# Kernel tuning notes

Hardware: AMD Instinct MI355X
Metric: run time of the kernel (lower is better)

The kernel has to match this reference:

```python
import jax, jax.numpy as jnp
import numpy as np
from jax import lax

SHIFT = 32  # shift_range from init
EPS_NORM = 1e-12
EPS_MASK = 1e-6


def _l2_normalize_flat(x):
    # F.normalize(x.reshape(B,-1)): per-sample L2 normalize with eps 1e-12
    B = x.shape[0]
    flat = x.reshape(B, -1)
    n = jnp.linalg.norm(flat, axis=1, keepdims=True)
    return (flat / jnp.maximum(n, EPS_NORM)).reshape(x.shape)


def setup_inputs() -> dict:
    key = jax.random.key(0)
    k1, k2 = jax.random.split(key)
    grd_feature = jax.random.normal(k1, (8, 32, 32, 32), dtype=jnp.float32)
    sat_feature = jax.random.normal(k2, (8, 32, 128, 128), dtype=jnp.float32)
    return {"grd_feature": grd_feature, "sat_feature": sat_feature, "test_method": 1}


def reference(grd_feature, sat_feature, test_method):
    # test_method == 1 path (default); test_method in {0,1} only differ in divisor
    M, C, H_s, W_s = sat_feature.shape
    N, _, H, W = grd_feature.shape
    kH = min(H, H_s - 2 * SHIFT)
    kW = min(W, W_s - 2 * SHIFT)

    # center-crop ground template to (kH, kW) and L2-normalize per sample
    gh0, gw0 = H // 2 - kH // 2, W // 2 - kW // 2
    grd = grd_feature[:, :, gh0:gh0 + 2 * (kH // 2), gw0:gw0 + 2 * (kW // 2)]
    N_, _, H_k, W_k = grd.shape
    grd = _l2_normalize_flat(grd)

    # center-crop satellite to search region and L2-normalize per sample
    sh0 = H_s // 2 - SHIFT - kH // 2
    sw0 = W_s // 2 - SHIFT - kW // 2
    sat = sat_feature[:, :, sh0:sh0 + 2 * (SHIFT + kH // 2), sw0:sw0 + 2 * (SHIFT + kW // 2)]
    _, _, H_i, W_i = sat.shape
    sat = _l2_normalize_flat(sat)

    # all-pairs cross-correlation: corr[m, n, y, x] (torch grouped-conv on repeated sat
    # is equivalent to a plain VALID conv of sat with all N ground filters)
    corr = lax.conv_general_dilated(
        sat, grd, window_strides=(1, 1), padding='VALID',
        dimension_numbers=('NCHW', 'OIHW', 'NCHW'))  # [M, N, Ho, Wo]
    Ho, Wo = corr.shape[2], corr.shape[3]

    # sliding-window sum of |sat|^2 (avg_pool with divisor_override=1, summed over C)
    s2 = jnp.sum(sat * sat, axis=1)  # [M, H_i, W_i]
    partical = lax.reduce_window(s2, jnp.float32(0), lax.add,
                                 (1, H_k, W_k), (1, 1, 1), 'VALID')  # [M, Ho, Wo]
    if test_method == 0:
        denom = jnp.sqrt(partical)
    else:
        denom = partical
    corr = corr / jnp.maximum(denom[:, None], EPS_NORM)

    similarity_matrix = jnp.max(corr, axis=(2, 3))  # [M, N]

    # diagonal pairs (m == n): peak localization
    diag = jnp.diagonal(corr, axis1=0, axis2=1)        # [Ho, Wo, M]
    diag = jnp.transpose(diag, (2, 0, 1)).reshape(M, -1)
    max_index = jnp.argmax(diag, axis=-1)
    pos_h = max_index // Wo
    pos_w = max_index % Wo

    grd_mask = (jnp.abs(jnp.sum(grd, axis=1)) > EPS_MASK).astype(jnp.float32)  # [N, H_k, W_k]

    def place(ph, pw, gm):
        z = jnp.zeros((1, H_i, W_i), dtype=jnp.float32)
        return lax.dynamic_update_slice(z, gm[None], (0, ph, pw))

    mask = jax.vmap(place)(pos_h, pos_w, grd_mask)  # [M, 1, H_i, W_i]
    return similarity_matrix, mask
```

## Files before the change

### kernel.cpp

```cpp
#include <hip/hip_runtime.h>
#include <stdint.h>

typedef unsigned short u16;
typedef unsigned int u32;
typedef unsigned long long u64;
typedef __bf16 bf16x8 __attribute__((ext_vector_type(8)));
typedef float floatx4 __attribute__((ext_vector_type(4)));

#define DEVI static __device__ __forceinline__

DEVI u16 f2bf(float f) {
  uint32_t u = __builtin_bit_cast(uint32_t, f);
  u += 0x7FFFu + ((u >> 16) & 1u);
  return (u16)(u >> 16);
}
DEVI float bf2f(u16 b) { return __builtin_bit_cast(float, (uint32_t)b << 16); }

DEVI u32 encf(float f) {
  u32 u = __builtin_bit_cast(u32, f);
  return (u >> 31) ? ~u : (u | 0x80000000u);
}
DEVI float decf(u32 e) {
  u32 u = (e >> 31) ? (e & 0x7FFFFFFFu) : ~e;
  return __builtin_bit_cast(float, u);
}

DEVI void cp16(const u16* g, u16* l) {
#if __has_builtin(__builtin_amdgcn_global_load_lds)
  __builtin_amdgcn_global_load_lds(
      (const __attribute__((address_space(1))) uint32_t*)g,
      (__attribute__((address_space(3))) uint32_t*)l, 16, 0, 0);
#else
  *(uint4*)l = *(const uint4*)g;
#endif
}

static constexpr size_t OFF_CORRP = 0;
static constexpr size_t OFF_SATT  = OFF_CORRP + (size_t)4*270400*4;
static constexpr size_t OFF_GRDP  = OFF_SATT + (size_t)8*4*96*96*8*2;
static constexpr size_t OFF_S2    = OFF_GRDP + (size_t)4*1024*16*8*2;
static constexpr size_t OFF_PART  = OFF_S2   + (size_t)73728*4;
static constexpr size_t OFF_NRMP  = OFF_PART + (size_t)33800*4;
static constexpr size_t OFF_GNRM  = OFF_NRMP + 768*4;
static constexpr size_t OFF_MASK  = OFF_GNRM + 32;
static constexpr size_t OFF_PMAX  = OFF_MASK + (size_t)8192*4;
static constexpr size_t OFF_CNT   = OFF_PMAX + 320*4;
static constexpr size_t OFF_CAND  = OFF_CNT  + 512;

__global__ __launch_bounds__(256) void k_prep(
    const float* __restrict__ grd, const float* __restrict__ sat,
    u16* __restrict__ sTh, u16* __restrict__ gP,
    float* __restrict__ s2, float* __restrict__ nrmp,
    float* __restrict__ gnrm, float* __restrict__ gmask,
    u32* __restrict__ cnts) {
  __shared__ float L[32*100];
  __shared__ float red[256];
  const int t = threadIdx.x;
  if (blockIdx.x < 768) {
    const int m = blockIdx.x / 96, y = blockIdx.x - (blockIdx.x / 96) * 96;
    #pragma unroll
    for (int k = 0; k < 3; ++k) {
      const int idx = k*256 + t;
      const int c = idx / 24, xq = idx - c*24;
      const float4 v = *(const float4*)(sat + (((size_t)m*32 + c)*128 + (16+y))*128 + 16 + xq*4);
      *(float4*)(&L[c*100 + xq*4]) = v;
    }
    __syncthreads();
    float ss = 0.f;
    if (t < 96) {
      #pragma unroll
      for (int c = 0; c < 32; ++c) { const float v = L[c*100 + t]; ss += v*v; }
      s2[(size_t)m*9216 + y*96 + t] = ss;
    }
    red[t] = ss; __syncthreads();
    for (int s = 128; s > 0; s >>= 1) { if (t < s) red[t] += red[t+s]; __syncthreads(); }
    if (t == 0) nrmp[m*96 + y] = red[0];
    for (int idx = t; idx < 384; idx += 256) {
      const int cb = idx / 96, x = idx - cb*96;
      union { u16 us[8]; uint4 v4; } P;
      #pragma unroll
      for (int e = 0; e < 8; ++e) P.us[e] = f2bf(L[(cb*8+e)*100 + x]);
      *(uint4*)(&sTh[(((size_t)m*4+cb)*9216 + (size_t)y*96 + x)*8]) = P.v4;
    }
  } else if (blockIdx.x == 776) {
    if (t < 72) cnts[t] = 0u;
  } else {
    const int n = blockIdx.x - 768;
    float nn = 0.f, scs[4];
    #pragma unroll
    for (int it = 0; it < 4; ++it) {
      const int pidx = it*256 + t;
      float vals[32]; float sc = 0.f;
      #pragma unroll
      for (int c = 0; c < 32; ++c) {
        const float v = grd[((size_t)n*32 + c)*1024 + pidx];
        vals[c] = v; sc += v; nn += v*v;
      }
      scs[it] = sc;
      #pragma unroll
      for (int cb = 0; cb < 4; ++cb) {
        union { u16 us[8]; uint4 v4; } ph, pl;
        #pragma unroll
        for (int e = 0; e < 8; ++e) {
          const float v = vals[cb*8+e];
          const u16 h = f2bf(v); ph.us[e] = h; pl.us[e] = f2bf(v - bf2f(h));
        }
        const size_t o = ((size_t)cb*1024 + pidx)*128;
        *(uint4*)(&gP[o + (size_t)n*8])     = ph.v4;
        *(uint4*)(&gP[o + (size_t)(n+8)*8]) = pl.v4;
      }
    }
    red[t] = nn; __syncthreads();
    for (int s = 128; s > 0; s >>= 1) { if (t < s) red[t] += red[t+s]; __syncthreads(); }
    const float gn = fmaxf(sqrtf(red[0]), 1e-12f);
    if (t == 0) gnrm[n] = red[0];
    const float thr = 1e-6f * gn;
    #pragma unroll
    for (int it = 0; it < 4; ++it)
      gmask[n*1024 + it*256 + t] = (fabsf(scs[it]) > thr) ? 1.f : 0.f;
  }
}

__global__ __launch_bounds__(256, 3) void k_conv(
    const u16* __restrict__ satT, const u16* __restrict__ gP,
    const float* __restrict__ s2, float* __restrict__ corr_p,
    float* __restrict__ part)
{
  __shared__ __align__(16) u16 patch[41*48*8];

  const int bi = blockIdx.x;
  const int tid = threadIdx.x;

  if (bi >= 1056) {
    float* S  = (float*)patch;
    float* HS = S + 40*96;
    const int pb = bi - 1056;
    const int pm = pb / 9, ysl = (pb - pm*9)*8;
    const int nrows = (65 - ysl) < 8 ? (65 - ysl) : 8;
    const int scnt  = (96 - ysl) < 40 ? (96 - ysl) : 40;
    for (int idx = tid; idx < scnt*96; idx += 256)
      S[idx] = s2[(size_t)pm*9216 + (size_t)ysl*96 + idx];
    __syncthreads();
    const int hrows = nrows + 31;
    for (int idx = tid; idx < hrows*65; idx += 256) {
      const int r = idx / 65, xo = idx - r*65;
      const float* p = &S[r*96 + xo];
      float s = 0.f;
      #pragma unroll
      for (int j = 0; j < 32; ++j) s += p[j];
      HS[idx] = s;
    }
    __syncthreads();
    for (int idx = tid; idx < nrows*65; idx += 256) {
      const int r = idx / 65, xo = idx - r*65;
      float s = 0.f;
      #pragma unroll
      for (int i = 0; i < 32; ++i) s += HS[(r+i)*65 + xo];
      part[(size_t)pm*4225 + (size_t)(ysl+r)*65 + xo] = s;
    }
    return;
  }

  const int wave = tid >> 6, lane = tid & 63;
  const int pr = lane & 15, q = lane >> 4;

  if (bi >= 896) {
    const int e = bi - 896;
    const int cb = e & 3;
    const int yt = (e >> 2) % 5;
    const int m  = e / 20;
    const int ybase = yt * 13;
    const size_t rowbase = ((size_t)(m*4 + cb) * 96 + ybase) * 96;
    for (int k = tid; k < 44*32; k += 256) {
      const int rho = k >> 5, px = k & 31;
      cp16(&satT[(rowbase + (size_t)rho*96 + 64 + px)*8], &patch[(size_t)k*8]);
    }
    asm volatile("s_waitcnt vmcnt(0)" ::: "memory");
    __syncthreads();
    const int prc = pr < 13 ? pr : 12;
    floatx4 acc = (floatx4){0.f, 0.f, 0.f, 0.f};
    #pragma unroll
    for (int jbi = 0; jbi < 2; ++jbi) {
      const int jb = wave*2 + jbi;
      const int px_e = jb*4 + q;
      const u16* bp = gP + ((size_t)cb*1024 + (size_t)(jb*4+q))*128 + (size_t)pr*8;
      uint4 Br[8];
      #pragma unroll
      for (int ii = 0; ii < 8; ++ii) Br[ii] = *(const uint4*)(bp + (size_t)ii*4096);
      uint4 Ah[8];
      #pragma unroll
      for (int s = 0; s < 6; ++s)
        Ah[s] = *(const uint4*)(&patch[((size_t)(prc + s)*32 + px_e)*8]);
      #pragma unroll
      for (int i = 0; i < 32; ++i) {
        if (i < 26)
          Ah[(i+6)&7] = *(const uint4*)(&patch[((size_t)(prc + i + 6)*32 + px_e)*8]);
        const bf16x8 bf = __builtin_bit_cast(bf16x8, Br[i&7]);
        if (i < 24)
          Br[(i+8)&7] = *(const uint4*)(bp + (size_t)(i+8)*4096);
        acc = __builtin_amdgcn_mfma_f32_16x16x32_bf16(
            __builtin_bit_cast(bf16x8, Ah[i&7]), bf, acc, 0, 0, 0);
      }
    }
    float v4[4];
    #pragma unroll
    for (int k = 0; k < 4; ++k) v4[k] = acc[k] + __shfl_xor(acc[k], 8);
    __syncthreads();
    float* red = (float*)patch;
    #pragma unroll
    for (int k = 0; k < 4; ++k) red[((size_t)wave*64 + lane)*5 + k] = v4[k];
    __syncthreads();
    if (wave == 0 && pr < 8) {
      #pragma unroll
      for (int k = 0; k < 4; ++k) {
        const int yoff = q*4 + k;
        if (yoff < 13) {
          float s = 0.f;
          #pragma unroll
          for (int w = 0; w < 4; ++w) s += red[((size_t)w*64 + lane)*5 + k];
          corr_p[(size_t)cb*270400 + ((size_t)(m*8+pr)*65 + (ybase+yoff))*65 + 64] = s;
        }
      }
    }
    return;
  }

  int b = bi;
  const int cb = b & 3; b >>= 2;
  const int xt = b & 3; b >>= 2;
  const int yt = b % 7;
  const int m  = b / 7;
  const int x0 = xt*16;

  if (yt < 6) {
    const int y0 = yt*10;
    const size_t rowbase = ((size_t)(m*4 + cb) * 96 + y0) * 96;
    for (int k = tid; k < 41*48; k += 256) {
      const int rho = k / 48, px = k - (k/48)*48;
      cp16(&satT[(rowbase + (size_t)rho*96 + x0 + px)*8], &patch[(size_t)k*8]);
    }
    asm volatile("s_waitcnt vmcnt(0)" ::: "memory");
    __syncthreads();

    floatx4 acc[10];
    #pragma unroll
    for (int r = 0; r < 10; ++r) acc[r] = (floatx4){0.f, 0.f, 0.f, 0.f};

    #pragma unroll
    for (int jbi = 0; jbi < 2; ++jbi) {
      const int jb = wave*2 + jbi;
      const int apx = pr + jb*4 + q;
      const u16* bp = gP + ((size_t)cb*1024 + (size_t)(jb*4+q))*128 + (size_t)pr*8;

      uint4 Br[8];
      #pragma unroll
      for (int ii = 0; ii < 8; ++ii) Br[ii] = *(const uint4*)(bp + (size_t)ii*4096);
      uint4 Ah[12];
      #pragma unroll
      for (int s = 0; s < 12; ++s) Ah[s] = *(const uint4*)(&patch[((size_t)s*48 + apx)*8]);

      #pragma unroll
      for (int i = 0; i < 32; ++i) {
        const bf16x8 bf = __builtin_bit_cast(bf16x8, Br[i&7]);
        if (i < 24)
          Br[(i+8)&7] = *(const uint4*)(bp + (size_t)(i+8)*4096);
        #pragma unroll
        for (int r = 0; r < 10; ++r)
          acc[r] = __builtin_amdgcn_mfma_f32_16x16x32_bf16(
              __builtin_bit_cast(bf16x8, Ah[(i+r)%12]), bf, acc[r], 0, 0, 0);
        if (i < 29)
          Ah[(i+12)%12] = *(const uint4*)(&patch[((size_t)(i+12)*48 + apx)*8]);
      }
    }

    float vals[40];
    #pragma unroll
    for (int r = 0; r < 10; ++r)
      #pragma unroll
      for (int k = 0; k < 4; ++k)
        vals[r*4+k] = acc[r][k] + __shfl_xor(acc[r][k], 8);

    float* red = (float*)patch;
    #pragma unroll
    for (int half = 0; half < 2; ++half) {
      __syncthreads();
      #pragma unroll
      for (int u = 0; u < 20; ++u) red[((size_t)wave*64 + lane)*21 + u] = vals[half*20 + u];
      __syncthreads();
      if (wave == 0 && pr < 8) {
        #pragma unroll
        for (int r = 0; r < 5; ++r) {
          #pragma unroll
          for (int k = 0; k < 4; ++k) {
            const int x = x0 + q*4 + k;
            float s = 0.f;
            #pragma unroll
            for (int w = 0; w < 4; ++w) s += red[((size_t)w*64 + lane)*21 + r*4 + k];
            corr_p[(size_t)cb*270400 + ((size_t)(m*8+pr)*65 + (y0 + half*5 + r))*65 + x] = s;
          }
        }
      }
    }
  } else {
    const int y0 = 60;
    const size_t rowbase = ((size_t)(m*4 + cb) * 96 + y0) * 96;
    for (int k = tid; k < 36*48; k += 256) {
      const int rho = k / 48, px = k - (k/48)*48;
      cp16(&satT[(rowbase + (size_t)rho*96 + x0 + px)*8], &patch[(size_t)k*8]);
    }
    asm volatile("s_waitcnt vmcnt(0)" ::: "memory");
    __syncthreads();

    floatx4 acc[5];
    #pragma unroll
    for (int r = 0; r < 5; ++r) acc[r] = (floatx4){0.f, 0.f, 0.f, 0.f};

    #pragma unroll
    for (int jbi = 0; jbi < 2; ++jbi) {
      const int jb = wave*2 + jbi;
      const int apx = pr + jb*4 + q;
      const u16* bp = gP + ((size_t)cb*1024 + (size_t)(jb*4+q))*128 + (size_t)pr*8;

      uint4 Br[8];
      #pragma unroll
      for (int ii = 0; ii < 8; ++ii) Br[ii] = *(const uint4*)(bp + (size_t)ii*4096);
      uint4 Ah[8];
      #pragma unroll
      for (int s = 0; s < 6; ++s) Ah[s] = *(const uint4*)(&patch[((size_t)s*48 + apx)*8]);

      #pragma unroll
      for (int i = 0; i < 32; ++i) {
        if (i < 30)
          Ah[(i+6)&7] = *(const uint4*)(&patch[((size_t)(i+6)*48 + apx)*8]);
        const bf16x8 bf = __builtin_bit_cast(bf16x8, Br[i&7]);
        if (i < 24)
          Br[(i+8)&7] = *(const uint4*)(bp + (size_t)(i+8)*4096);
        #pragma unroll
        for (int r = 0; r < 5; ++r)
          acc[r] = __builtin_amdgcn_mfma_f32_16x16x32_bf16(
              __builtin_bit_cast(bf16x8, Ah[(i+r)&7]), bf, acc[r], 0, 0, 0);
      }
    }

    float vals[20];
    #pragma unroll
    for (int r = 0; r < 5; ++r)
      #pragma unroll
      for (int k = 0; k < 4; ++k)
        vals[r*4+k] = acc[r][k] + __shfl_xor(acc[r][k], 8);

    __syncthreads();
    float* red = (float*)patch;
    #pragma unroll
    for (int u = 0; u < 20; ++u) red[((size_t)wave*64 + lane)*21 + u] = vals[u];
    __syncthreads();
    if (wave == 0 && pr < 8) {
      #pragma unroll
      for (int r = 0; r < 5; ++r) {
        #pragma unroll
        for (int k = 0; k < 4; ++k) {
          const int x = x0 + q*4 + k;
          float s = 0.f;
          #pragma unroll
          for (int w = 0; w < 4; ++w) s += red[((size_t)w*64 + lane)*21 + r*4 + k];
          corr_p[(size_t)cb*270400 + ((size_t)(m*8+pr)*65 + (y0+r))*65 + x] = s;
        }
      }
    }
  }
}

__global__ __launch_bounds__(256) void k_post(
    const float* __restrict__ corr_p, const float* __restrict__ part,
    const float* __restrict__ nrmp, const float* __restrict__ gnrm,
    const int* __restrict__ tm, const float* __restrict__ grd,
    const float* __restrict__ sat, const float* __restrict__ gmask,
    u32* __restrict__ pmaxE, u32* __restrict__ grpcnt,
    u32* __restrict__ candcnt, u64* __restrict__ cand,
    float* __restrict__ out)
{
  __shared__ float red[256];
  __shared__ float s_bcast;
  __shared__ int s_last;
  __shared__ int fidx[128];
  __shared__ u32 fcnt;

  const int bi = blockIdx.x;
  const int m = bi / 40, n = (bi / 5) & 7, yc = bi % 5, g = m*8 + n;
  const int t = threadIdx.x;
  const bool diag = (m == n);

  red[t] = (t < 96) ? nrmp[m*96 + t] : 0.f;
  __syncthreads();
  for (int s = 128; s > 0; s >>= 1) { if (t < s) red[t] += red[t+s]; __syncthreads(); }
  const float srn = 1.f / fmaxf(sqrtf(red[0]), 1e-12f);
  const float grn = 1.f / fmaxf(sqrtf(gnrm[n]), 1e-12f);
  const float cscale = grn * srn, pscale = srn * srn;
  const int method = tm[0];

  const float* cp = corr_p + (size_t)g*4225;
  const float* pp = part + (size_t)m*4225;
  const int i0 = yc*845, i1 = i0 + 845;
  float vv[4];
  float bestv = -3.4e38f;
  #pragma unroll
  for (int k = 0; k < 4; ++k) {
    const int idx = i0 + k*256 + t;
    float v = -3.4e38f;
    if (idx < i1) {
      const float c = cp[idx] + cp[idx+270400] + cp[idx+540800] + cp[idx+811200];
      const float pt = pp[idx] * pscale;
      float denom = (method == 0) ? sqrtf(pt) : pt;
      denom = fmaxf(denom, 1e-12f);
      v = c * cscale / denom;
    }
    vv[k] = v;
    bestv = fmaxf(bestv, v);
  }
  __syncthreads();
  red[t] = bestv; __syncthreads();
  for (int s = 128; s > 0; s >>= 1) { if (t < s) red[t] = fmaxf(red[t], red[t+s]); __syncthreads(); }
  if (t == 0) { s_bcast = red[0]; atomicExch(&pmaxE[bi], encf(red[0])); }
  __syncthreads();
  if (diag) {
    const float lthr = s_bcast - 3e-3f;
    #pragma unroll
    for (int k = 0; k < 4; ++k) {
      const int idx = i0 + k*256 + t;
      if (idx < i1 && vv[k] >= lthr) {
        const u32 s = atomicAdd(&candcnt[n], 1u);
        if (s < 128)
          atomicExch(&cand[n*128 + s],
                     ((u64)__builtin_bit_cast(u32, vv[k]) << 32) | (u32)idx);
      }
    }
  }
  __syncthreads();
  if (t == 0) s_last = (atomicAdd(&grpcnt[g], 1u) == 4u) ? 1 : 0;
  __syncthreads();
  if (!s_last) return;

  if (t == 0) {
    float gm = -3.4e38f;
    #pragma unroll
    for (int k = 0; k < 5; ++k) gm = fmaxf(gm, decf(atomicOr(&pmaxE[g*5 + k], 0u)));
    out[g] = gm;
    s_bcast = gm;
  }
  __syncthreads();
  if (!diag) return;

  const float gmax = s_bcast;
  const float thr = gmax - 3e-3f;
  if (t == 0) fcnt = 0u;
  __syncthreads();
  u32 nc = atomicAdd(&candcnt[n], 0u); if (nc > 128) nc = 128;
  if (t < (int)nc) {
    const u64 pk = atomicAdd(&cand[n*128 + t], 0ULL);
    const float vf = __builtin_bit_cast(float, (u32)(pk >> 32));
    const int idx = (int)(u32)pk;
    if (vf >= thr) { const u32 s = atomicAdd(&fcnt, 1u); fidx[s] = idx; }
  }
  __syncthreads();
  if (t == 0 && fcnt == 0u) { fidx[0] = 0; fcnt = 1u; }
  __syncthreads();
  const int nf = (int)fcnt;

  __shared__ float sbest; __shared__ int sbix;
  if (t == 0) { sbest = -3.4e38f; sbix = 0x7FFFFFFF; }
  __syncthreads();
  const int c = t >> 3, s8 = t & 7;
  for (int ci = 0; ci < nf; ++ci) {
    const int idx = fidx[ci];
    const int y = idx / 65, x = idx - y*65;
    float a = 0.f;
    #pragma unroll
    for (int ii = 0; ii < 4; ++ii) {
      const int i = s8 + ii*8;
      const float* gr = grd + ((size_t)n*32 + c)*1024 + i*32;
      const float* sr = sat + (((size_t)n*32 + c)*128 + (16 + y + i))*128 + (16 + x);
      #pragma unroll
      for (int j = 0; j < 32; ++j) a += gr[j] * sr[j];
    }
    red[t] = a; __syncthreads();
    for (int st = 128; st > 0; st >>= 1) { if (t < st) red[t] += red[t+st]; __syncthreads(); }
    if (t == 0) {
      const float pt = part[(size_t)n*4225 + idx] * pscale;
      float denom = (method == 0) ? sqrtf(pt) : pt;
      denom = fmaxf(denom, 1e-12f);
      const float v = red[0] * cscale / denom;
      if (v > sbest || (v == sbest && idx < sbix)) { sbest = v; sbix = idx; }
    }
    __syncthreads();
  }
  const int bix = sbix;
  const int ph = bix / 65, pw = bix - (bix/65)*65;
  for (int p = t; p < 9216; p += 256) {
    const int yy = p / 96, xx = p - yy*96;
    float val = 0.f;
    if (yy >= ph && yy < ph+32 && xx >= pw && xx < pw+32)
      val = gmask[n*1024 + (yy-ph)*32 + (xx-pw)];
    out[64 + (size_t)n*9216 + p] = val;
  }
}

extern "C" void kernel_launch(void* const* d_in, const int* in_sizes, int n_in,
                              void* d_out, int out_size, void* d_ws, size_t ws_size,
                              hipStream_t stream) {
  const float* grd = (const float*)d_in[0];
  const float* sat = (const float*)d_in[1];
  const int*   tm  = (const int*)d_in[2];
  float* out = (float*)d_out;
  char* ws = (char*)d_ws;

  float* corrp = (float*)(ws + OFF_CORRP);
  u16*   sTh   = (u16*)(ws + OFF_SATT);
  u16*   gP    = (u16*)(ws + OFF_GRDP);
  float* s2    = (float*)(ws + OFF_S2);
  float* part  = (float*)(ws + OFF_PART);
  float* nrmp  = (float*)(ws + OFF_NRMP);
  float* gnrm  = (float*)(ws + OFF_GNRM);
  float* gmask = (float*)(ws + OFF_MASK);
  u32*   pmaxE = (u32*)(ws + OFF_PMAX);
  u32*   cnts  = (u32*)(ws + OFF_CNT);
  u64*   cand  = (u64*)(ws + OFF_CAND);

  k_prep<<<777,  256, 0, stream>>>(grd, sat, sTh, gP, s2, nrmp, gnrm, gmask, cnts);
  k_conv<<<1128, 256, 0, stream>>>(sTh, gP, s2, corrp, part);
  k_post<<<320,  256, 0, stream>>>(corrp, part, nrmp, gnrm, tm, grd, sat, gmask,
                                   pmaxE, cnts, cnts + 64, cand, out);
}
```

Before: 147.6 us.

## Fuse post-processing into conv kernel with per-sample completion counters and spin-wait

Removes the separate k_post launch. The post work (max reduction, candidate refinement, mask placement) now runs in the trailing partial-sum blocks of k_conv. Those blocks spin-wait on per-sample atomic counters until all 132 conv blocks and all 9 partial blocks for that sample have finished. This saves a kernel launch and the cross-block candidate exchange. In exchange, only 64 blocks do the post work, each handling a whole 65x65 map. Correctness also depends on the waiting blocks being scheduled after, or alongside, the producer blocks, which risks deadlock or stalls.

```diff
diff --git a/kernel.cpp b/kernel.cpp
--- a/kernel.cpp
+++ b/kernel.cpp
@@ -15,15 +15,6 @@
   return (u16)(u >> 16);
 }
 DEVI float bf2f(u16 b) { return __builtin_bit_cast(float, (uint32_t)b << 16); }
-
-DEVI u32 encf(float f) {
-  u32 u = __builtin_bit_cast(u32, f);
-  return (u >> 31) ? ~u : (u | 0x80000000u);
-}
-DEVI float decf(u32 e) {
-  u32 u = (e >> 31) ? (e & 0x7FFFFFFFu) : ~e;
-  return __builtin_bit_cast(float, u);
-}
 
 DEVI void cp16(const u16* g, u16* l) {
 #if __has_builtin(__builtin_amdgcn_global_load_lds)
@@ -43,9 +34,7 @@
 static constexpr size_t OFF_NRMP  = OFF_PART + (size_t)33800*4;
 static constexpr size_t OFF_GNRM  = OFF_NRMP + 768*4;
 static constexpr size_t OFF_MASK  = OFF_GNRM + 32;
-static constexpr size_t OFF_PMAX  = OFF_MASK + (size_t)8192*4;
-static constexpr size_t OFF_CNT   = OFF_PMAX + 320*4;
-static constexpr size_t OFF_CAND  = OFF_CNT  + 512;
+static constexpr size_t OFF_CNT   = OFF_MASK + (size_t)8192*4;
 
 __global__ __launch_bounds__(256) void k_prep(
     const float* __restrict__ grd, const float* __restrict__ sat,
@@ -83,7 +72,7 @@
       *(uint4*)(&sTh[(((size_t)m*4+cb)*9216 + (size_t)y*96 + x)*8]) = P.v4;
     }
   } else if (blockIdx.x == 776) {
-    if (t < 72) cnts[t] = 0u;
+    if (t < 16) cnts[t] = 0u;
   } else {
     const int n = blockIdx.x - 768;
     float nn = 0.f, scs[4];
@@ -124,39 +113,136 @@
 __global__ __launch_bounds__(256, 3) void k_conv(
     const u16* __restrict__ satT, const u16* __restrict__ gP,
     const float* __restrict__ s2, float* __restrict__ corr_p,
-    float* __restrict__ part)
+    float* __restrict__ part, const float* __restrict__ nrmp,
+    const float* __restrict__ gnrm, const int* __restrict__ tm,
+    const float* __restrict__ grd, const float* __restrict__ sat,
+    const float* __restrict__ gmask, u32* __restrict__ cnts,
+    float* __restrict__ out)
 {
   __shared__ __align__(16) u16 patch[41*48*8];
+  __shared__ float sbest; __shared__ int sbix;
+  __shared__ u32 fcnt;
 
   const int bi = blockIdx.x;
   const int tid = threadIdx.x;
 
   if (bi >= 1056) {
-    float* S  = (float*)patch;
-    float* HS = S + 40*96;
+    float* F = (float*)patch;
     const int pb = bi - 1056;
-    const int pm = pb / 9, ysl = (pb - pm*9)*8;
-    const int nrows = (65 - ysl) < 8 ? (65 - ysl) : 8;
-    const int scnt  = (96 - ysl) < 40 ? (96 - ysl) : 40;
-    for (int idx = tid; idx < scnt*96; idx += 256)
-      S[idx] = s2[(size_t)pm*9216 + (size_t)ysl*96 + idx];
-    __syncthreads();
-    const int hrows = nrows + 31;
-    for (int idx = tid; idx < hrows*65; idx += 256) {
-      const int r = idx / 65, xo = idx - r*65;
-      const float* p = &S[r*96 + xo];
-      float s = 0.f;
-      #pragma unroll
-      for (int j = 0; j < 32; ++j) s += p[j];
-      HS[idx] = s;
-    }
-    __syncthreads();
-    for (int idx = tid; idx < nrows*65; idx += 256) {
-      const int r = idx / 65, xo = idx - r*65;
-      float s = 0.f;
-      #pragma unroll
-      for (int i = 0; i < 32; ++i) s += HS[(r+i)*65 + xo];
-      part[(size_t)pm*4225 + (size_t)(ysl+r)*65 + xo] = s;
+    const int pm = pb / 9, j = pb - pm*9;
+    {
+      float* S  = F;
+      float* HS = F + 40*96;
+      const int ysl = j*8;
+      const int nrows = (65 - ysl) < 8 ? (65 - ysl) : 8;
+      const int scnt  = (96 - ysl) < 40 ? (96 - ysl) : 40;
+      for (int idx = tid; idx < scnt*96; idx += 256)
+        S[idx] = s2[(size_t)pm*9216 + (size_t)ysl*96 + idx];
+      __syncthreads();
+      const int hrows = nrows + 31;
+      for (int idx = tid; idx < hrows*65; idx += 256) {
+        const int r = idx / 65, xo = idx - r*65;
+        const float* p = &S[r*96 + xo];
+        float s = 0.f;
+        #pragma unroll
+        for (int jj = 0; jj < 32; ++jj) s += p[jj];
+        HS[idx] = s;
+      }
+      __syncthreads();
+      for (int idx = tid; idx < nrows*65; idx += 256) {
+        const int r = idx / 65, xo = idx - r*65;
+        float s = 0.f;
+        #pragma unroll
+        for (int i = 0; i < 32; ++i) s += HS[(r+i)*65 + xo];
+        part[(size_t)pm*4225 + (size_t)(ysl+r)*65 + xo] = s;
+      }
+    }
+    __threadfence();
+    __syncthreads();
+    if (tid == 0) atomicAdd(&cnts[8+pm], 1u);
+    if (j >= 8) return;
+
+    const int n = j;
+    if (tid == 0) {
+      while (atomicAdd(&cnts[pm], 0u) < 132u || atomicAdd(&cnts[8+pm], 0u) < 9u)
+        __builtin_amdgcn_s_sleep(8);
+    }
+    __syncthreads();
+    __threadfence();
+
+    float* vbuf = F;
+    float* red  = F + 4608;
+    int*  fidx  = (int*)(F + 4880);
+
+    red[tid] = (tid < 96) ? nrmp[pm*96 + tid] : 0.f;
+    __syncthreads();
+    for (int s = 128; s > 0; s >>= 1) { if (tid < s) red[tid] += red[tid+s]; __syncthreads(); }
+    const float srn = 1.f / fmaxf(sqrtf(red[0]), 1e-12f);
+    const float grn = 1.f / fmaxf(sqrtf(gnrm[n]), 1e-12f);
+    const float cscale = grn * srn, pscale = srn * srn;
+    const int method = tm[0];
+    const bool diag = (pm == n);
+    const float* cp = corr_p + (size_t)(pm*8+n)*4225;
+    const float* pp = part + (size_t)pm*4225;
+    __syncthreads();
+
+    float bestv = -3.4e38f;
+    for (int idx = tid; idx < 4225; idx += 256) {
+      const float c = cp[idx] + cp[idx+270400] + cp[idx+540800] + cp[idx+811200];
+      const float pt = pp[idx] * pscale;
+      float denom = (method == 0) ? sqrtf(pt) : pt;
+      denom = fmaxf(denom, 1e-12f);
+      const float v = c * cscale / denom;
+      if (diag) vbuf[idx] = v;
+      bestv = fmaxf(bestv, v);
+    }
+    __syncthreads();
+    red[tid] = bestv; __syncthreads();
+    for (int s = 128; s > 0; s >>= 1) { if (tid < s) red[tid] = fmaxf(red[tid], red[tid+s]); __syncthreads(); }
+    if (tid == 0) out[pm*8 + n] = red[0];
+    if (!diag) return;
+    const float vmax = red[0];
+
+    if (tid == 0) { fcnt = 0u; sbest = -3.4e38f; sbix = 0x7FFFFFFF; }
+    __syncthreads();
+    const float thr = vmax - 3e-3f;
+    for (int idx = tid; idx < 4225; idx += 256)
+      if (vbuf[idx] >= thr) { const u32 s = atomicAdd(&fcnt, 1u); if (s < 128) fidx[s] = idx; }
+    __syncthreads();
+    int nf = (int)fcnt; if (nf > 128) nf = 128; if (nf < 1) nf = 1;
+
+    const int c = tid >> 3, s8 = tid & 7;
+    for (int ci = 0; ci < nf; ++ci) {
+      const int idx = fidx[ci];
+      const int y = idx / 65, x = idx - y*65;
+      float a = 0.f;
+      #pragma unroll
+      for (int ii = 0; ii < 4; ++ii) {
+        const int i = s8 + ii*8;
+        const float* gr = grd + ((size_t)n*32 + c)*1024 + i*32;
+        const float* sr = sat + (((size_t)n*32 + c)*128 + (16 + y + i))*128 + (16 + x);
+        #pragma unroll
+        for (int jj = 0; jj < 32; ++jj) a += gr[jj] * sr[jj];
+      }
+      red[tid] = a; __syncthreads();
+      for (int st = 128; st > 0; st >>= 1) { if (tid < st) red[tid] += red[tid+st]; __syncthreads(); }
+      if (tid == 0) {
+        const float pt = pp[idx] * pscale;
+        float denom = (method == 0) ? sqrtf(pt) : pt;
+        denom = fmaxf(denom, 1e-12f);
+        const float v = red[0] * cscale / denom;
+        if (v > sbest || (v == sbest && idx < sbix)) { sbest = v; sbix = idx; }
+      }
+      __syncthreads();
+    }
+    const int bix = sbix;
+    const int ph = bix / 65, pw = bix - (bix/65)*65;
+    for (int p = tid; p < 9216; p += 256) {
+      const int yy = p / 96, xx = p - yy*96;
+      float val = 0.f;
+      if (yy >= ph && yy < ph+32 && xx >= pw && xx < pw+32)
+        val = gmask[n*1024 + (yy-ph)*32 + (xx-pw)];
+      out[64 + (size_t)n*9216 + p] = val;
     }
     return;
   }
@@ -222,6 +308,9 @@
         }
       }
     }
+    __threadfence();
+    __syncthreads();
+    if (tid == 0) atomicAdd(&cnts[m], 1u);
     return;
   }
 
@@ -368,140 +457,9 @@
       }
     }
   }
-}
-
-__global__ __launch_bounds__(256) void k_post(
-    const float* __restrict__ corr_p, const float* __restrict__ part,
-    const float* __restrict__ nrmp, const float* __restrict__ gnrm,
-    const int* __restrict__ tm, const float* __restrict__ grd,
-    const float* __restrict__ sat, const float* __restrict__ gmask,
-    u32* __restrict__ pmaxE, u32* __restrict__ grpcnt,
-    u32* __restrict__ candcnt, u64* __restrict__ cand,
-    float* __restrict__ out)
-{
-  __shared__ float red[256];
-  __shared__ float s_bcast;
-  __shared__ int s_last;
-  __shared__ int fidx[128];
-  __shared__ u32 fcnt;
-
-  const int bi = blockIdx.x;
-  const int m = bi / 40, n = (bi / 5) & 7, yc = bi % 5, g = m*8 + n;
-  const int t = threadIdx.x;
-  const bool diag = (m == n);
-
-  red[t] = (t < 96) ? nrmp[m*96 + t] : 0.f;
+  __threadfence();
   __syncthreads();
-  for (int s = 128; s > 0; s >>= 1) { if (t < s) red[t] += red[t+s]; __syncthreads(); }
-  const float srn = 1.f / fmaxf(sqrtf(red[0]), 1e-12f);
-  const float grn = 1.f / fmaxf(sqrtf(gnrm[n]), 1e-12f);
-  const float cscale = grn * srn, pscale = srn * srn;
-  const int method = tm[0];
-
-  const float* cp = corr_p + (size_t)g*4225;
-  const float* pp = part + (size_t)m*4225;
-  const int i0 = yc*845, i1 = i0 + 845;
-  float vv[4];
-  float bestv = -3.4e38f;
-  #pragma unroll
-  for (int k = 0; k < 4; ++k) {
-    const int idx = i0 + k*256 + t;
-    float v = -3.4e38f;
-    if (idx < i1) {
-      const float c = cp[idx] + cp[idx+270400] + cp[idx+540800] + cp[idx+811200];
-      const float pt = pp[idx] * pscale;
-      float denom = (method == 0) ? sqrtf(pt) : pt;
-      denom = fmaxf(denom, 1e-12f);
-      v = c * cscale / denom;
-    }
-    vv[k] = v;
-    bestv = fmaxf(bestv, v);
-  }
-  __syncthreads();
-  red[t] = bestv; __syncthreads();
-  for (int s = 128; s > 0; s >>= 1) { if (t < s) red[t] = fmaxf(red[t], red[t+s]); __syncthreads(); }
-  if (t == 0) { s_bcast = red[0]; atomicExch(&pmaxE[bi], encf(red[0])); }
-  __syncthreads();
-  if (diag) {
-    const float lthr = s_bcast - 3e-3f;
-    #pragma unroll
-    for (int k = 0; k < 4; ++k) {
-      const int idx = i0 + k*256 + t;
-      if (idx < i1 && vv[k] >= lthr) {
-        const u32 s = atomicAdd(&candcnt[n], 1u);
-        if (s < 128)
-          atomicExch(&cand[n*128 + s],
-                     ((u64)__builtin_bit_cast(u32, vv[k]) << 32) | (u32)idx);
-      }
-    }
-  }
-  __syncthreads();
-  if (t == 0) s_last = (atomicAdd(&grpcnt[g], 1u) == 4u) ? 1 : 0;
-  __syncthreads();
-  if (!s_last) return;
-
-  if (t == 0) {
-    float gm = -3.4e38f;
-    #pragma unroll
-    for (int k = 0; k < 5; ++k) gm = fmaxf(gm, decf(atomicOr(&pmaxE[g*5 + k], 0u)));
-    out[g] = gm;
-    s_bcast = gm;
-  }
-  __syncthreads();
-  if (!diag) return;
-
-  const float gmax = s_bcast;
-  const float thr = gmax - 3e-3f;
-  if (t == 0) fcnt = 0u;
-  __syncthreads();
-  u32 nc = atomicAdd(&candcnt[n], 0u); if (nc > 128) nc = 128;
-  if (t < (int)nc) {
-    const u64 pk = atomicAdd(&cand[n*128 + t], 0ULL);
-    const float vf = __builtin_bit_cast(float, (u32)(pk >> 32));
-    const int idx = (int)(u32)pk;
-    if (vf >= thr) { const u32 s = atomicAdd(&fcnt, 1u); fidx[s] = idx; }
-  }
-  __syncthreads();
-  if (t == 0 && fcnt == 0u) { fidx[0] = 0; fcnt = 1u; }
-  __syncthreads();
-  const int nf = (int)fcnt;
-
-  __shared__ float sbest; __shared__ int sbix;
-  if (t == 0) { sbest = -3.4e38f; sbix = 0x7FFFFFFF; }
-  __syncthreads();
-  const int c = t >> 3, s8 = t & 7;
-  for (int ci = 0; ci < nf; ++ci) {
-    const int idx = fidx[ci];
-    const int y = idx / 65, x = idx - y*65;
-    float a = 0.f;
-    #pragma unroll
-    for (int ii = 0; ii < 4; ++ii) {
-      const int i = s8 + ii*8;
-      const float* gr = grd + ((size_t)n*32 + c)*1024 + i*32;
-      const float* sr = sat + (((size_t)n*32 + c)*128 + (16 + y + i))*128 + (16 + x);
-      #pragma unroll
-      for (int j = 0; j < 32; ++j) a += gr[j] * sr[j];
-    }
-    red[t] = a; __syncthreads();
-    for (int st = 128; st > 0; st >>= 1) { if (t < st) red[t] += red[t+st]; __syncthreads(); }
-    if (t == 0) {
-      const float pt = part[(size_t)n*4225 + idx] * pscale;
-      float denom = (method == 0) ? sqrtf(pt) : pt;
-      denom = fmaxf(denom, 1e-12f);
-      const float v = red[0] * cscale / denom;
-      if (v > sbest || (v == sbest && idx < sbix)) { sbest = v; sbix = idx; }
-    }
-    __syncthreads();
-  }
-  const int bix = sbix;
-  const int ph = bix / 65, pw = bix - (bix/65)*65;
-  for (int p = t; p < 9216; p += 256) {
-    const int yy = p / 96, xx = p - yy*96;
-    float val = 0.f;
-    if (yy >= ph && yy < ph+32 && xx >= pw && xx < pw+32)
-      val = gmask[n*1024 + (yy-ph)*32 + (xx-pw)];
-    out[64 + (size_t)n*9216 + p] = val;
-  }
+  if (tid == 0) atomicAdd(&cnts[m], 1u);
 }
 
 extern "C" void kernel_launch(void* const* d_in, const int* in_sizes, int n_in,
@@ -521,12 +479,9 @@
   float* nrmp  = (float*)(ws + OFF_NRMP);
   float* gnrm  = (float*)(ws + OFF_GNRM);
   float* gmask = (float*)(ws + OFF_MASK);
-  u32*   pmaxE = (u32*)(ws + OFF_PMAX);
   u32*   cnts  = (u32*)(ws + OFF_CNT);
-  u64*   cand  = (u64*)(ws + OFF_CAND);
 
   k_prep<<<777,  256, 0, stream>>>(grd, sat, sTh, gP, s2, nrmp, gnrm, gmask, cnts);
-  k_conv<<<1128, 256, 0, stream>>>(sTh, gP, s2, corrp, part);
-  k_post<<<320,  256, 0, stream>>>(corrp, part, nrmp, gnrm, tm, grd, sat, gmask,
-                                   pmaxE, cnts, cnts + 64, cand, out);
+  k_conv<<<1128, 256, 0, stream>>>(sTh, gP, s2, corrp, part, nrmp, gnrm, tm,
+                                   grd, sat, gmask, cnts, out);
 }
```

Result: slower. 272.1 us (+84.4%).
